# Kernel optimization log

Hardware: AMD Instinct MI355X
Metric: run time of the kernel (lower is better)

## Reference

```python
import jax, jax.numpy as jnp
import numpy as np

SCALE = 0.02  # weight init scale to keep activations sane


def setup_inputs() -> dict:
    key = jax.random.key(0)
    ks = jax.random.split(key, 6)
    B, T, C = 4, 2048, 2048
    NB, BS, R = 16, 128, 128  # n_diag_blocks, diag_blocksize, rank
    x = jax.random.normal(ks[0], (B, T, C), dtype=jnp.float32)
    diag = jax.random.normal(ks[1], (4, NB, BS, BS), dtype=jnp.float32) * SCALE
    left_w = jax.random.normal(ks[2], (4, R, C), dtype=jnp.float32) * SCALE   # Linear(in=C, out=R).weight
    right_w = jax.random.normal(ks[3], (4, C, R), dtype=jnp.float32) * SCALE  # Linear(in=R, out=C).weight
    right_b = jax.random.normal(ks[4], (4, C), dtype=jnp.float32) * SCALE
    bias_p = jax.random.normal(ks[5], (4, C), dtype=jnp.float32) * SCALE
    return {"x": x, "diag": diag, "left_w": left_w, "right_w": right_w,
            "right_b": right_b, "bias_p": bias_p, "n_head": 16}


def _lori_fc(x, diag_i, left_i, right_w_i, right_b_i, bias_i):
    # x: [B,T,C]; block-diagonal path done as batched per-block matmul
    B, T, C = x.shape
    nb, bs, _ = diag_i.shape
    x1 = jnp.einsum('btnd,nde->btne', x.reshape(B, T, nb, bs), diag_i).reshape(B, T, C)
    # low-rank path: right(left(x)) with right bias
    x2 = jnp.einsum('btr,cr->btc', jnp.einsum('btc,rc->btr', x, left_i), right_w_i) + right_b_i
    return x1 + x2 + bias_i  # module's own bias (bias=True)


def reference(x, diag, left_w, right_w, right_b, bias_p, n_head):
    B, T, C = x.shape
    hd = C // n_head
    q = _lori_fc(x, diag[0], left_w[0], right_w[0], right_b[0], bias_p[0])
    k = _lori_fc(x, diag[1], left_w[1], right_w[1], right_b[1], bias_p[1])
    v = _lori_fc(x, diag[2], left_w[2], right_w[2], right_b[2], bias_p[2])
    # [B, H, T, hd]
    q = q.reshape(B, T, n_head, hd).transpose(0, 2, 1, 3)
    k = k.reshape(B, T, n_head, hd).transpose(0, 2, 1, 3)
    v = v.reshape(B, T, n_head, hd).transpose(0, 2, 1, 3)
    att = jnp.einsum('bhqd,bhkd->bhqk', q, k) * (1.0 / jnp.sqrt(jnp.float32(hd)))
    causal = jnp.tril(jnp.ones((T, T), dtype=bool))
    att = jnp.where(causal, att, jnp.finfo(att.dtype).min)
    att = jax.nn.softmax(att, axis=-1)
    y = jnp.einsum('bhqk,bhkd->bhqd', att, v)
    y = y.transpose(0, 2, 1, 3).reshape(B, T, C)
    y = _lori_fc(y, diag[3], left_w[3], right_w[3], right_b[3], bias_p[3])
    return y
```

## Files before the change

### kernel.cpp

```cpp
#include <hip/hip_runtime.h>

typedef short bf16x8 __attribute__((ext_vector_type(8)));
typedef short bf16x4 __attribute__((ext_vector_type(4)));
typedef float f32x4  __attribute__((ext_vector_type(4)));

#define AS1 __attribute__((address_space(1)))
#define AS3 __attribute__((address_space(3)))

__device__ __forceinline__ void gload16(const void* g, void* l) {
  __builtin_amdgcn_global_load_lds((const AS1 void*)g, (AS3 void*)l, 16, 0, 0);
}

__device__ __forceinline__ short f2bf(float f) {
  union { float fv; unsigned u; } v; v.fv = f;
  unsigned r = v.u + 0x7fffu + ((v.u >> 16) & 1u);
  return (short)(r >> 16);
}

__device__ __forceinline__ short f2bf_t(float f) {
  return (short)(__float_as_uint(f) >> 16);
}

__global__ void cast_x_kernel(const float* __restrict__ x, short* __restrict__ xb, long n4) {
  long i = (long)blockIdx.x * 256 + threadIdx.x;
  if (i < n4) {
    float4 v = ((const float4*)x)[i];
    short4 s;
    s.x = f2bf(v.x); s.y = f2bf(v.y); s.z = f2bf(v.z); s.w = f2bf(v.w);
    ((short4*)xb)[i] = s;
  }
}

__global__ void prep_kernel(const float* __restrict__ left_w, const float* __restrict__ diag,
                            const float* __restrict__ right_w,
                            short* __restrict__ LT, short* __restrict__ WT) {
  long idx = (long)blockIdx.x * 256 + threadIdx.x;
  const long LTN = 4L * 128 * 2048;
  const long WTN = 4L * 16 * 128 * 256;
  if (idx < LTN) {
    LT[idx] = f2bf(left_w[idx]);
  } else if (idx < LTN + WTN) {
    long j = idx - LTN;
    int d = (int)(j & 255);
    long rest = j >> 8;
    int e = (int)(rest & 127);
    long gi = rest >> 7;
    int i = (int)(gi >> 4), n = (int)(gi & 15);
    float v;
    if (d < 128) v = diag[(gi * 128 + d) * 128 + e];
    else         v = right_w[((long)i * 2048 + n * 128 + e) * 128 + (d - 128)];
    WT[j] = f2bf(v);
  }
}

__global__ __launch_bounds__(256) void gemm_bt(const short* __restrict__ A, const short* __restrict__ BT,
                                               short* __restrict__ C, int M, int N, int K) {
  __shared__ __align__(16) short As[128 * 64];
  __shared__ __align__(16) short Bs[128 * 64];
  int tid = threadIdx.x, w = tid >> 6, lane = tid & 63;
  int m0 = blockIdx.x * 128, n0 = blockIdx.y * 128;
  int wm = (w >> 1) * 64, wn = (w & 1) * 64;
  int quad = lane >> 4, l16 = lane & 15;
  int srow = lane >> 3;
  int schunk = ((lane & 7) ^ srow) * 8;
  f32x4 acc[4][4] = {};
  for (int k0 = 0; k0 < K; k0 += 64) {
    for (int p = 0; p < 4; ++p) {
      int r = p * 32 + w * 8 + srow;
      gload16(&A[(long)(m0 + r) * K + k0 + schunk], &As[(p * 32 + w * 8) * 64]);
      gload16(&BT[(long)(n0 + r) * K + k0 + schunk], &Bs[(p * 32 + w * 8) * 64]);
    }
    __syncthreads();
#pragma unroll
    for (int kk = 0; kk < 2; ++kk) {
      int c = (((kk * 4 + quad) ^ (l16 & 7)) * 8);
      bf16x8 a[4], b[4];
#pragma unroll
      for (int t = 0; t < 4; ++t) a[t] = *(const bf16x8*)&As[(wm + t * 16 + l16) * 64 + c];
#pragma unroll
      for (int t = 0; t < 4; ++t) b[t] = *(const bf16x8*)&Bs[(wn + t * 16 + l16) * 64 + c];
#pragma unroll
      for (int mt = 0; mt < 4; ++mt)
#pragma unroll
        for (int nt = 0; nt < 4; ++nt)
          acc[mt][nt] = __builtin_amdgcn_mfma_f32_16x16x32_bf16(a[mt], b[nt], acc[mt][nt], 0, 0, 0);
    }
    __syncthreads();
  }
#pragma unroll
  for (int mt = 0; mt < 4; ++mt)
#pragma unroll
    for (int nt = 0; nt < 4; ++nt)
#pragma unroll
      for (int r = 0; r < 4; ++r) {
        int m = m0 + wm + mt * 16 + quad * 4 + r;
        int n = n0 + wn + nt * 16 + l16;
        C[(long)m * N + n] = f2bf(acc[mt][nt][r]);
      }
}

__global__ __launch_bounds__(256) void lori_gemm(const short* __restrict__ tok, const short* __restrict__ rnk,
                                                 int rstride, const short* __restrict__ WT,
                                                 const float* __restrict__ rb, const float* __restrict__ bp,
                                                 int i_base, short* __restrict__ qb, short* __restrict__ kb,
                                                 short* __restrict__ vT, float* __restrict__ out) {
  __shared__ __align__(16) short As[128 * 64];
  __shared__ __align__(16) short Bs[128 * 64];
  int tid = threadIdx.x, w = tid >> 6, lane = tid & 63;
  int i = i_base + (blockIdx.y >> 4);
  int n = blockIdx.y & 15;
  int t0 = blockIdx.x * 128;
  int co = (i < 3) ? i * 128 : 0;
  const short* WTn = WT + (long)(i * 16 + n) * 128 * 256;
  int wm = (w >> 1) * 64, wn = (w & 1) * 64;
  int quad = lane >> 4, l16 = lane & 15;
  int srow = lane >> 3;
  int schunk = ((lane & 7) ^ srow) * 8;
  f32x4 acc[4][4] = {};
#pragma unroll
  for (int kt = 0; kt < 4; ++kt) {
    for (int p = 0; p < 4; ++p) {
      int r = p * 32 + w * 8 + srow;
      const short* ga;
      if (kt < 2) ga = &tok[(long)(t0 + r) * 2048 + n * 128 + kt * 64 + schunk];
      else        ga = &rnk[(long)(t0 + r) * rstride + co + (kt - 2) * 64 + schunk];
      gload16(ga, &As[(p * 32 + w * 8) * 64]);
      gload16(&WTn[r * 256 + kt * 64 + schunk], &Bs[(p * 32 + w * 8) * 64]);
    }
    __syncthreads();
#pragma unroll
    for (int kk = 0; kk < 2; ++kk) {
      int c = (((kk * 4 + quad) ^ (l16 & 7)) * 8);
      bf16x8 a[4], b[4];
#pragma unroll
      for (int t = 0; t < 4; ++t) a[t] = *(const bf16x8*)&As[(wm + t * 16 + l16) * 64 + c];
#pragma unroll
      for (int t = 0; t < 4; ++t) b[t] = *(const bf16x8*)&Bs[(wn + t * 16 + l16) * 64 + c];
#pragma unroll
      for (int mt = 0; mt < 4; ++mt)
#pragma unroll
        for (int nt = 0; nt < 4; ++nt)
          acc[mt][nt] = __builtin_amdgcn_mfma_f32_16x16x32_bf16(a[mt], b[nt], acc[mt][nt], 0, 0, 0);
    }
    __syncthreads();
  }
  int b = t0 >> 11;
  int tl0 = t0 & 2047;
  const float QSC = 0.08838834764831845f * 1.4426950408889634f;
#pragma unroll
  for (int mt = 0; mt < 4; ++mt) {
#pragma unroll
    for (int nt = 0; nt < 4; ++nt) {
      int e = wn + nt * 16 + l16;
      int c = n * 128 + e;
      float bias = rb[i * 2048 + c] + bp[i * 2048 + c];
      int tl = tl0 + wm + mt * 16 + quad * 4;
      if (i == 0) {
#pragma unroll
        for (int r = 0; r < 4; ++r)
          qb[((long)(b * 16 + n) * 2048 + tl + r) * 128 + e] = f2bf((acc[mt][nt][r] + bias) * QSC);
      } else if (i == 1) {
#pragma unroll
        for (int r = 0; r < 4; ++r)
          kb[((long)(b * 16 + n) * 2048 + tl + r) * 128 + e] = f2bf(acc[mt][nt][r] + bias);
      } else if (i == 2) {
        short4 s4;
        s4.x = f2bf(acc[mt][nt][0] + bias);
        s4.y = f2bf(acc[mt][nt][1] + bias);
        s4.z = f2bf(acc[mt][nt][2] + bias);
        s4.w = f2bf(acc[mt][nt][3] + bias);
        *(short4*)&vT[((long)(b * 16 + n) * 128 + e) * 2048 + tl] = s4;
      } else {
#pragma unroll
        for (int r = 0; r < 4; ++r)
          out[(long)(t0 + wm + mt * 16 + quad * 4 + r) * 2048 + c] = acc[mt][nt][r] + bias;
      }
    }
  }
}

__global__ __launch_bounds__(512, 3) void attn_kernel(const short* __restrict__ qb, const short* __restrict__ kb,
                                                      const short* __restrict__ vT, short* __restrict__ y) {
  __shared__ __align__(16) short ks[2][64 * 128];
  __shared__ __align__(16) short vs[2][128 * 64];
  int tid = threadIdx.x, w = tid >> 6, lane = tid & 63;
  int id = blockIdx.x;
  int xcd = id & 7;
  int sl = (id >> 3) & 31;
  int round = id >> 8;
  int bh = xcd + 8 * (sl & 7);
  int qt = round ? (sl >> 3) : 7 - (sl >> 3);
  int b = bh >> 4, h = bh & 15;
  int quad = lane >> 4, l16 = lane & 15;

  bf16x8 aq[2][4];
#pragma unroll
  for (int mt = 0; mt < 2; ++mt)
#pragma unroll
    for (int kk = 0; kk < 4; ++kk)
      aq[mt][kk] = *(const bf16x8*)&qb[((long)bh * 2048 + qt * 256 + w * 32 + mt * 16 + l16) * 128 + kk * 32 + quad * 8];

  f32x4 O[2][8] = {};
  f32x4 Lacc[2] = {};
  float mst[2] = {-3.0e38f, -3.0e38f};
  const bf16x4 ones4 = {(short)0x3F80, (short)0x3F80, (short)0x3F80, (short)0x3F80};

  int kq = lane >> 4;
  int kchunk = l16 ^ ((w * 4 + kq) & 15);
  int vrow8 = lane >> 3;
  int vchunk = (lane & 7) ^ (vrow8 & 7);

  const short* kbase = kb + (long)bh * 2048 * 128;
  const short* vbase = vT + (long)bh * 128 * 2048;

#define STAGE(JT, BUF) {                                                              \
    for (int p = 0; p < 2; ++p) {                                                     \
      int r = p * 32 + w * 4 + kq;                                                    \
      gload16(&kbase[((long)((JT) * 64 + r)) * 128 + kchunk * 8], &ks[BUF][(p * 32 + w * 4) * 128]); \
      int r2 = p * 64 + w * 8 + vrow8;                                                \
      gload16(&vbase[(long)r2 * 2048 + (JT) * 64 + vchunk * 8], &vs[BUF][(p * 64 + w * 8) * 64]);    \
    }                                                                                 \
  }

  int jmax_w = 4 * qt + (w >> 1);
  int jtend = 4 * qt + 3;
  STAGE(0, 0)
  __syncthreads();
  for (int jt = 0; jt <= jtend; ++jt) {
    int cur = jt & 1;
    if (jt < jtend) STAGE(jt + 1, cur ^ 1)

    if (jt <= jmax_w) {
      f32x4 s[2][4] = {};
#pragma unroll
      for (int nt = 0; nt < 4; ++nt)
#pragma unroll
        for (int kk = 0; kk < 4; ++kk) {
          bf16x8 bk = *(const bf16x8*)&ks[cur][(nt * 16 + l16) * 128 + (((kk * 4 + quad) ^ l16) * 8)];
          s[0][nt] = __builtin_amdgcn_mfma_f32_16x16x32_bf16(bk, aq[0][kk], s[0][nt], 0, 0, 0);
          s[1][nt] = __builtin_amdgcn_mfma_f32_16x16x32_bf16(bk, aq[1][kk], s[1][nt], 0, 0, 0);
        }
      if (jt == jmax_w) {
#pragma unroll
        for (int mt = 0; mt < 2; ++mt)
#pragma unroll
          for (int nt = 0; nt < 4; ++nt) {
            int q = qt * 256 + w * 32 + mt * 16 + l16;
#pragma unroll
            for (int r = 0; r < 4; ++r) {
              int key = jt * 64 + nt * 16 + quad * 4 + r;
              if (key > q) s[mt][nt][r] = -3.0e38f;
            }
          }
      }
      bf16x4 pb[2][4];
#pragma unroll
      for (int mt = 0; mt < 2; ++mt) {
        f32x4 vm;
#pragma unroll
        for (int r = 0; r < 4; ++r)
          vm[r] = fmaxf(fmaxf(s[mt][0][r], s[mt][1][r]), fmaxf(s[mt][2][r], s[mt][3][r]));
        float mx = fmaxf(fmaxf(vm[0], vm[1]), fmaxf(vm[2], vm[3]));
        mx = fmaxf(mx, __shfl_xor(mx, 16));
        mx = fmaxf(mx, __shfl_xor(mx, 32));
        float nm = fmaxf(mst[mt], mx);
        float al = __builtin_amdgcn_exp2f(mst[mt] - nm);
        mst[mt] = nm;
        Lacc[mt] *= al;
#pragma unroll
        for (int dt = 0; dt < 8; ++dt) O[mt][dt] *= al;
#pragma unroll
        for (int nt = 0; nt < 4; ++nt) {
          bf16x4 p;
#pragma unroll
          for (int r = 0; r < 4; ++r) p[r] = f2bf_t(__builtin_amdgcn_exp2f(s[mt][nt][r] - nm));
          pb[mt][nt] = p;
        }
      }
#pragma unroll
      for (int nt = 0; nt < 4; ++nt) {
        int coff = ((nt * 2 + (quad >> 1)) ^ (l16 & 7)) * 8 + (quad & 1) * 4;
        bf16x4 av[8];
#pragma unroll
        for (int dt = 0; dt < 8; ++dt) av[dt] = *(const bf16x4*)&vs[cur][(dt * 16 + l16) * 64 + coff];
#pragma unroll
        for (int mt = 0; mt < 2; ++mt) {
#pragma unroll
          for (int dt = 0; dt < 8; ++dt)
            O[mt][dt] = __builtin_amdgcn_mfma_f32_16x16x16bf16_1k(av[dt], pb[mt][nt], O[mt][dt], 0, 0, 0);
          Lacc[mt] = __builtin_amdgcn_mfma_f32_16x16x16bf16_1k(ones4, pb[mt][nt], Lacc[mt], 0, 0, 0);
        }
      }
    }
    __syncthreads();
  }
#undef STAGE
#pragma unroll
  for (int mt = 0; mt < 2; ++mt) {
    float inv = __builtin_amdgcn_rcpf(Lacc[mt][0]);
    int q = qt * 256 + w * 32 + mt * 16 + l16;
#pragma unroll
    for (int dt = 0; dt < 8; ++dt) {
      short4 s4;
      s4.x = f2bf(O[mt][dt][0] * inv);
      s4.y = f2bf(O[mt][dt][1] * inv);
      s4.z = f2bf(O[mt][dt][2] * inv);
      s4.w = f2bf(O[mt][dt][3] * inv);
      *(short4*)&y[((long)(b * 2048 + q)) * 2048 + h * 128 + dt * 16 + quad * 4] = s4;
    }
  }
}

extern "C" void kernel_launch(void* const* d_in, const int* in_sizes, int n_in,
                              void* d_out, int out_size, void* d_ws, size_t ws_size,
                              hipStream_t stream) {
  const float* x       = (const float*)d_in[0];
  const float* diag    = (const float*)d_in[1];
  const float* left_w  = (const float*)d_in[2];
  const float* right_w = (const float*)d_in[3];
  const float* right_b = (const float*)d_in[4];
  const float* bias_p  = (const float*)d_in[5];
  float* out = (float*)d_out;

  char* ws = (char*)d_ws;
  short* xb = (short*)(ws + 0);
  short* LT = (short*)(ws + 33554432);
  short* WT = (short*)(ws + 35651584);
  short* xl = (short*)(ws + 39845888);
  short* yl = (short*)(ws + 46137344);
  short* qb = (short*)(ws + 48234496);
  short* kb = (short*)(ws + 81788928);
  short* vT = (short*)(ws + 115343360);
  short* y  = xb;

  cast_x_kernel<<<16384, 256, 0, stream>>>(x, xb, 4194304L);
  prep_kernel<<<12288, 256, 0, stream>>>(left_w, diag, right_w, LT, WT);
  gemm_bt<<<dim3(64, 3), 256, 0, stream>>>(xb, LT, xl, 8192, 384, 2048);
  lori_gemm<<<dim3(64, 48), 256, 0, stream>>>(xb, xl, 384, WT, right_b, bias_p, 0, qb, kb, vT, nullptr);
  attn_kernel<<<dim3(512), 512, 0, stream>>>(qb, kb, vT, y);
  gemm_bt<<<dim3(64, 1), 256, 0, stream>>>(y, LT + 3L * 128 * 2048, yl, 8192, 128, 2048);
  lori_gemm<<<dim3(64, 16), 256, 0, stream>>>(y, yl, 128, WT, right_b, bias_p, 3, nullptr, nullptr, nullptr, out);
}
```

Baseline: 453.8 us.

## Double-buffer LDS in GEMM kernels and merge cast/prep launches

Both the low-rank projection GEMM and the LoRI block GEMM now use two LDS buffers, so the global-to-LDS load of the next K tile is issued before the MFMA work on the current tile. This hides global load latency behind compute and removes one barrier per iteration. The x cast kernel and the weight prep kernel are merged into a single launch to save launch overhead. Doubling the LDS to 64KB per block may lower occupancy.

```diff
diff --git a/kernel.cpp b/kernel.cpp
--- a/kernel.cpp
+++ b/kernel.cpp
@@ -21,26 +21,23 @@
   return (short)(__float_as_uint(f) >> 16);
 }
 
-__global__ void cast_x_kernel(const float* __restrict__ x, short* __restrict__ xb, long n4) {
-  long i = (long)blockIdx.x * 256 + threadIdx.x;
-  if (i < n4) {
-    float4 v = ((const float4*)x)[i];
+__global__ void cast_prep_kernel(const float* __restrict__ x, const float* __restrict__ left_w,
+                                 const float* __restrict__ diag, const float* __restrict__ right_w,
+                                 short* __restrict__ xb, short* __restrict__ LT, short* __restrict__ WT) {
+  long idx = (long)blockIdx.x * 256 + threadIdx.x;
+  const long N4 = 4194304L;
+  const long LTN = 4L * 128 * 2048;
+  const long WTN = 4L * 16 * 128 * 256;
+  if (idx < N4) {
+    float4 v = ((const float4*)x)[idx];
     short4 s;
     s.x = f2bf(v.x); s.y = f2bf(v.y); s.z = f2bf(v.z); s.w = f2bf(v.w);
-    ((short4*)xb)[i] = s;
-  }
-}
-
-__global__ void prep_kernel(const float* __restrict__ left_w, const float* __restrict__ diag,
-                            const float* __restrict__ right_w,
-                            short* __restrict__ LT, short* __restrict__ WT) {
-  long idx = (long)blockIdx.x * 256 + threadIdx.x;
-  const long LTN = 4L * 128 * 2048;
-  const long WTN = 4L * 16 * 128 * 256;
-  if (idx < LTN) {
-    LT[idx] = f2bf(left_w[idx]);
-  } else if (idx < LTN + WTN) {
-    long j = idx - LTN;
+    ((short4*)xb)[idx] = s;
+  } else if (idx < N4 + LTN) {
+    long j = idx - N4;
+    LT[j] = f2bf(left_w[j]);
+  } else if (idx < N4 + LTN + WTN) {
+    long j = idx - N4 - LTN;
     int d = (int)(j & 255);
     long rest = j >> 8;
     int e = (int)(rest & 127);
@@ -55,30 +52,38 @@
 
 __global__ __launch_bounds__(256) void gemm_bt(const short* __restrict__ A, const short* __restrict__ BT,
                                                short* __restrict__ C, int M, int N, int K) {
-  __shared__ __align__(16) short As[128 * 64];
-  __shared__ __align__(16) short Bs[128 * 64];
+  __shared__ __align__(16) short As[2][128 * 64];
+  __shared__ __align__(16) short Bs[2][128 * 64];
   int tid = threadIdx.x, w = tid >> 6, lane = tid & 63;
   int m0 = blockIdx.x * 128, n0 = blockIdx.y * 128;
   int wm = (w >> 1) * 64, wn = (w & 1) * 64;
   int quad = lane >> 4, l16 = lane & 15;
   int srow = lane >> 3;
   int schunk = ((lane & 7) ^ srow) * 8;
+
+#define GSTAGE(K0, BUF) {                                                             \
+    for (int p = 0; p < 4; ++p) {                                                     \
+      int r = p * 32 + w * 8 + srow;                                                  \
+      gload16(&A[(long)(m0 + r) * K + (K0) + schunk], &As[BUF][(p * 32 + w * 8) * 64]); \
+      gload16(&BT[(long)(n0 + r) * K + (K0) + schunk], &Bs[BUF][(p * 32 + w * 8) * 64]); \
+    }                                                                                 \
+  }
+
   f32x4 acc[4][4] = {};
-  for (int k0 = 0; k0 < K; k0 += 64) {
-    for (int p = 0; p < 4; ++p) {
-      int r = p * 32 + w * 8 + srow;
-      gload16(&A[(long)(m0 + r) * K + k0 + schunk], &As[(p * 32 + w * 8) * 64]);
-      gload16(&BT[(long)(n0 + r) * K + k0 + schunk], &Bs[(p * 32 + w * 8) * 64]);
-    }
-    __syncthreads();
+  GSTAGE(0, 0)
+  __syncthreads();
+  int nk = K >> 6;
+  for (int it = 0; it < nk; ++it) {
+    int cur = it & 1;
+    if (it + 1 < nk) GSTAGE((it + 1) * 64, cur ^ 1)
 #pragma unroll
     for (int kk = 0; kk < 2; ++kk) {
       int c = (((kk * 4 + quad) ^ (l16 & 7)) * 8);
       bf16x8 a[4], b[4];
 #pragma unroll
-      for (int t = 0; t < 4; ++t) a[t] = *(const bf16x8*)&As[(wm + t * 16 + l16) * 64 + c];
-#pragma unroll
-      for (int t = 0; t < 4; ++t) b[t] = *(const bf16x8*)&Bs[(wn + t * 16 + l16) * 64 + c];
+      for (int t = 0; t < 4; ++t) a[t] = *(const bf16x8*)&As[cur][(wm + t * 16 + l16) * 64 + c];
+#pragma unroll
+      for (int t = 0; t < 4; ++t) b[t] = *(const bf16x8*)&Bs[cur][(wn + t * 16 + l16) * 64 + c];
 #pragma unroll
       for (int mt = 0; mt < 4; ++mt)
 #pragma unroll
@@ -87,6 +92,7 @@
     }
     __syncthreads();
   }
+#undef GSTAGE
 #pragma unroll
   for (int mt = 0; mt < 4; ++mt)
 #pragma unroll
@@ -104,8 +110,8 @@
                                                  const float* __restrict__ rb, const float* __restrict__ bp,
                                                  int i_base, short* __restrict__ qb, short* __restrict__ kb,
                                                  short* __restrict__ vT, float* __restrict__ out) {
-  __shared__ __align__(16) short As[128 * 64];
-  __shared__ __align__(16) short Bs[128 * 64];
+  __shared__ __align__(16) short As[2][128 * 64];
+  __shared__ __align__(16) short Bs[2][128 * 64];
   int tid = threadIdx.x, w = tid >> 6, lane = tid & 63;
   int i = i_base + (blockIdx.y >> 4);
   int n = blockIdx.y & 15;
@@ -116,26 +122,33 @@
   int quad = lane >> 4, l16 = lane & 15;
   int srow = lane >> 3;
   int schunk = ((lane & 7) ^ srow) * 8;
+
+#define LSTAGE(KT, BUF) {                                                             \
+    for (int p = 0; p < 4; ++p) {                                                     \
+      int r = p * 32 + w * 8 + srow;                                                  \
+      const short* ga;                                                                \
+      if ((KT) < 2) ga = &tok[(long)(t0 + r) * 2048 + n * 128 + (KT) * 64 + schunk];  \
+      else          ga = &rnk[(long)(t0 + r) * rstride + co + ((KT) - 2) * 64 + schunk]; \
+      gload16(ga, &As[BUF][(p * 32 + w * 8) * 64]);                                   \
+      gload16(&WTn[r * 256 + (KT) * 64 + schunk], &Bs[BUF][(p * 32 + w * 8) * 64]);   \
+    }                                                                                 \
+  }
+
   f32x4 acc[4][4] = {};
+  LSTAGE(0, 0)
+  __syncthreads();
 #pragma unroll
   for (int kt = 0; kt < 4; ++kt) {
-    for (int p = 0; p < 4; ++p) {
-      int r = p * 32 + w * 8 + srow;
-      const short* ga;
-      if (kt < 2) ga = &tok[(long)(t0 + r) * 2048 + n * 128 + kt * 64 + schunk];
-      else        ga = &rnk[(long)(t0 + r) * rstride + co + (kt - 2) * 64 + schunk];
-      gload16(ga, &As[(p * 32 + w * 8) * 64]);
-      gload16(&WTn[r * 256 + kt * 64 + schunk], &Bs[(p * 32 + w * 8) * 64]);
-    }
-    __syncthreads();
+    int cur = kt & 1;
+    if (kt < 3) LSTAGE(kt + 1, cur ^ 1)
 #pragma unroll
     for (int kk = 0; kk < 2; ++kk) {
       int c = (((kk * 4 + quad) ^ (l16 & 7)) * 8);
       bf16x8 a[4], b[4];
 #pragma unroll
-      for (int t = 0; t < 4; ++t) a[t] = *(const bf16x8*)&As[(wm + t * 16 + l16) * 64 + c];
-#pragma unroll
-      for (int t = 0; t < 4; ++t) b[t] = *(const bf16x8*)&Bs[(wn + t * 16 + l16) * 64 + c];
+      for (int t = 0; t < 4; ++t) a[t] = *(const bf16x8*)&As[cur][(wm + t * 16 + l16) * 64 + c];
+#pragma unroll
+      for (int t = 0; t < 4; ++t) b[t] = *(const bf16x8*)&Bs[cur][(wn + t * 16 + l16) * 64 + c];
 #pragma unroll
       for (int mt = 0; mt < 4; ++mt)
 #pragma unroll
@@ -144,6 +157,7 @@
     }
     __syncthreads();
   }
+#undef LSTAGE
   int b = t0 >> 11;
   int tl0 = t0 & 2047;
   const float QSC = 0.08838834764831845f * 1.4426950408889634f;
@@ -333,8 +347,7 @@
   short* vT = (short*)(ws + 115343360);
   short* y  = xb;
 
-  cast_x_kernel<<<16384, 256, 0, stream>>>(x, xb, 4194304L);
-  prep_kernel<<<12288, 256, 0, stream>>>(left_w, diag, right_w, LT, WT);
+  cast_prep_kernel<<<28672, 256, 0, stream>>>(x, left_w, diag, right_w, xb, LT, WT);
   gemm_bt<<<dim3(64, 3), 256, 0, stream>>>(xb, LT, xl, 8192, 384, 2048);
   lori_gemm<<<dim3(64, 48), 256, 0, stream>>>(xb, xl, 384, WT, right_b, bias_p, 0, qb, kb, vT, nullptr);
   attn_kernel<<<dim3(512), 512, 0, stream>>>(qb, kb, vT, y);
```

New measurement: 437.4 us. 1.04x faster.
